# Kernel tuning notes

Measured on AMD Instinct MI355X. Metric: run time of the kernel, lower is better.

## Reference

```python
import jax, jax.numpy as jnp
import numpy as np

IN_CH, OUT_CH, HID = 16, 16, 64
POS_DIM = 3
N_POINTS = 50000
N_EDGES = 800000
BATCH = 1

def setup_inputs() -> dict:
    key = jax.random.key(0)
    ks = jax.random.split(key, 10)
    x = jax.random.normal(ks[0], (BATCH, N_POINTS, IN_CH), dtype=jnp.float32)
    pos = jax.random.uniform(ks[1], (N_POINTS, POS_DIM), dtype=jnp.float32)
    edge_index = jax.random.randint(ks[2], (2, N_EDGES), 0, N_POINTS, dtype=jnp.int64)
    def lin(k, fan_in, fan_out):
        kw, kb = jax.random.split(k)
        bound = 1.0 / np.sqrt(fan_in)
        W = jax.random.uniform(kw, (fan_in, fan_out), minval=-bound, maxval=bound, dtype=jnp.float32)
        b = jax.random.uniform(kb, (fan_out,), minval=-bound, maxval=bound, dtype=jnp.float32)
        return W, b
    W1, b1 = lin(ks[3], 2 * POS_DIM, HID)
    Wh, bh = lin(ks[4], HID, HID)
    Wo, bo = lin(ks[5], HID, IN_CH * OUT_CH)
    return {"x": x, "pos": pos, "edge_index": edge_index,
            "W1": W1, "b1": b1, "Wh": Wh, "bh": bh, "Wo": Wo, "bo": bo}

def reference(x, pos, edge_index, W1, b1, Wh, bh, Wo, bo):
    gelu = lambda t: jax.nn.gelu(t, approximate=False)  # matches torch F.gelu default
    batch_size, n_points, in_ch = x.shape
    pos_flat = jnp.broadcast_to(pos[None], (batch_size,) + pos.shape).reshape(-1, pos.shape[-1])
    x_flat = x.reshape(-1, in_ch)
    src, dst = edge_index[0], edge_index[1]
    pos_enc = jnp.concatenate([pos_flat[src], pos_flat[dst]], axis=-1)  # [E, 2*pos_dim]
    h = gelu(pos_enc @ W1 + b1)
    h = gelu(h @ Wh + bh)
    h = h @ Wo + bo                                  # [E, in*out]
    kernel_weights = h.reshape(-1, in_ch, OUT_CH)    # [E, in, out]
    msg = jnp.einsum('eio,ei->eo', kernel_weights, x_flat[src])  # [E, out]
    out_flat = jax.ops.segment_sum(msg, dst, num_segments=batch_size * n_points)
    return out_flat.reshape(batch_size, n_points, OUT_CH)
```

## Files before the change

kernel.cpp:

```cpp
#include <hip/hip_runtime.h>

#define NPTS   50000
#define NEDGE  800000
#define NTILES 50000
#define NPAIRS 25000
#define NBLK   768
#define TOTW   (NBLK * 8)

typedef short  bf16x8 __attribute__((ext_vector_type(8)));
typedef float  f32x4  __attribute__((ext_vector_type(4)));
typedef int    i32x4  __attribute__((ext_vector_type(4)));
typedef unsigned short u16x8 __attribute__((ext_vector_type(8)));

__device__ __forceinline__ float gelu_tanh(float v) {
    float v2 = v * v;
    float u2 = v * fmaf(v2, 0.0713548162726f, 1.5957691216057f);
    float e  = __expf(u2);
    float r  = __builtin_amdgcn_rcpf(e + 1.0f);
    return v - v * r;
}

__device__ __forceinline__ short f2bf(float f) {
    unsigned u = __builtin_bit_cast(unsigned, f);
    unsigned r = (u + 0x7FFFu + ((u >> 16) & 1u)) >> 16;
    return (short)r;
}
__device__ __forceinline__ float bf2f(unsigned short h) {
    return __builtin_bit_cast(float, (unsigned)h << 16);
}

__device__ __forceinline__ int cvt_pk_bf16(float a, float b) {
    int r;
    asm("v_cvt_pk_bf16_f32 %0, %1, %2" : "=v"(r) : "v"(a), "v"(b));
    return r;
}

__device__ __forceinline__ int bperm(int addr, int v) {
    return __builtin_amdgcn_ds_bpermute(addr, v);
}
__device__ __forceinline__ int fbits(float v) { return __builtin_bit_cast(int, v); }
__device__ __forceinline__ float ibits(int v) { return __builtin_bit_cast(float, v); }

__global__ void zero_out_kernel(float* __restrict__ out, int n) {
    int i = blockIdx.x * blockDim.x + threadIdx.x;
    if (i < n) out[i] = 0.0f;
}

__global__ void xcopy_kernel(const float* __restrict__ x, unsigned short* __restrict__ xbf) {
    int i = blockIdx.x * 256 + threadIdx.x;
    if (i >= (NPTS * 16) / 4) return;
    float4 v = reinterpret_cast<const float4*>(x)[i];
    ushort4 o;
    o.x = (unsigned short)f2bf(v.x);
    o.y = (unsigned short)f2bf(v.y);
    o.z = (unsigned short)f2bf(v.z);
    o.w = (unsigned short)f2bf(v.w);
    reinterpret_cast<ushort4*>(xbf)[i] = o;
}

__global__ __launch_bounds__(512, 4) void edge_mfma_kernel(
    const unsigned short* __restrict__ xbf,
    const float* __restrict__ pos,
    const int*   __restrict__ ei,
    const float* __restrict__ W1,
    const float* __restrict__ b1,
    const float* __restrict__ Wh,
    const float* __restrict__ bh,
    const float* __restrict__ Wo,
    const float* __restrict__ bo,
    float* __restrict__ out)
{
    __shared__ bf16x8 WoF[32][64];
    __shared__ bf16x8 WhF[8][64];
    __shared__ bf16x8 W1F[4][64];
    __shared__ bf16x8 BOF[64];
    __shared__ float  bhs[64];

    const int tid = threadIdx.x;

#pragma unroll
    for (int p = 0; p < 4; ++p) {
        int e_id = p * 512 + tid;
        int s  = e_id >> 6;
        int l  = e_id & 63;
        int er_ = l & 15, g = l >> 4;
        int i  = s >> 1, kt = s & 1;
        int n  = i * 16 + er_;
        int kb = kt * 32 + g * 8;
        bf16x8 f;
#pragma unroll
        for (int j = 0; j < 8; ++j)
            f[j] = f2bf(Wo[(kb + j) * 256 + n]);
        WoF[s][l] = f;
    }
    {
        int s  = tid >> 6;
        int l  = tid & 63;
        int er_ = l & 15, g = l >> 4;
        int m  = s >> 1, kt = s & 1;
        int n  = m * 16 + er_;
        int kb = kt * 32 + g * 8;
        bf16x8 f;
#pragma unroll
        for (int j = 0; j < 8; ++j)
            f[j] = f2bf(Wh[(kb + j) * 64 + n]);
        WhF[s][l] = f;
    }
    if (tid < 256) {
        int m  = tid >> 6;
        int l  = tid & 63;
        int er_ = l & 15, g = l >> 4;
        int n  = m * 16 + er_;
        bf16x8 f;
#pragma unroll
        for (int j = 0; j < 8; ++j) {
            int k = g * 8 + j;
            float v = (k < 6) ? W1[k * 64 + n] : (k == 6 ? b1[n] : 0.0f);
            f[j] = f2bf(v);
        }
        W1F[m][l] = f;
    }
    if (tid < 64) {
        int er_ = tid & 15, g = tid >> 4;
        bf16x8 f;
#pragma unroll
        for (int j = 0; j < 8; ++j) {
            int i = g * 8 + j;
            f[j] = (g < 2) ? f2bf(bo[i * 16 + er_]) : (short)0;
        }
        BOF[tid] = f;
        bhs[tid] = bh[tid];
    }
    __syncthreads();

    const int wave = tid >> 6;
    const int lane = tid & 63;
    const int grp  = lane >> 4;
    const int er   = lane & 15;

    const int addrH0 = (er + (grp & 1) * 32) * 4;
    const int addrH1 = addrH0 + 64;
    const bool selHi = (grp >= 2);
    int addrT[4], addrD[4];
#pragma unroll
    for (int r = 0; r < 4; ++r) {
        addrT[r] = ((er >> 2) * 16 + grp * 4 + r) * 4;
        addrD[r] = (grp * 4 + r) * 4;
    }
    const int selT = er & 3;

    const bf16x8* wof = &WoF[0][lane];
    const bf16x8* whf = &WhF[0][lane];
    const bf16x8* w1f = &W1F[0][lane];
    const bf16x8  bofr = BOF[lane];
    const f32x4 zero = {0.f, 0.f, 0.f, 0.f};

    const int gwave = blockIdx.x * 8 + wave;

#pragma unroll 1
    for (int pr = gwave; pr < NPAIRS; pr += TOTW) {
        int sQ[2], dQ[2];
        bf16x8 apeQ[2];
        u16x8 xA[2], xB[2];
#pragma unroll
        for (int q = 0; q < 2; ++q) {
            const int eb = (2 * pr + q) << 4;
            int s = ei[eb + er];
            int d = ei[NEDGE + eb + er];
            s = min(max(s, 0), NPTS - 1);
            d = min(max(d, 0), NPTS - 1);
            sQ[q] = s; dQ[q] = d;

            const u16x8* xp = reinterpret_cast<const u16x8*>(xbf + (size_t)s * 16);
            xA[q] = xp[0];
            xB[q] = xp[1];

            float p0 = pos[s * 3 + 0], p1 = pos[s * 3 + 1], p2 = pos[s * 3 + 2];
            float p3 = pos[d * 3 + 0], p4 = pos[d * 3 + 1], p5 = pos[d * 3 + 2];
            const bool g0 = (grp == 0);
            bf16x8 ap;
            ap[0] = g0 ? f2bf(p0) : (short)0;
            ap[1] = g0 ? f2bf(p1) : (short)0;
            ap[2] = g0 ? f2bf(p2) : (short)0;
            ap[3] = g0 ? f2bf(p3) : (short)0;
            ap[4] = g0 ? f2bf(p4) : (short)0;
            ap[5] = g0 ? f2bf(p5) : (short)0;
            ap[6] = g0 ? (short)0x3F80 : (short)0;
            ap[7] = 0;
            apeQ[q] = ap;
        }

        float g1[2][4][4];
#pragma unroll
        for (int q = 0; q < 2; ++q)
#pragma unroll
            for (int m = 0; m < 4; ++m) {
                f32x4 c = __builtin_amdgcn_mfma_f32_16x16x32_bf16(w1f[m * 64], apeQ[q], zero, 0, 0, 0);
#pragma unroll
                for (int r = 0; r < 4; ++r) g1[q][m][r] = gelu_tanh(c[r]);
            }

        bf16x8 B2[2][2];
#pragma unroll
        for (int q = 0; q < 2; ++q)
#pragma unroll
            for (int kt = 0; kt < 2; ++kt) {
                int pk0[2], pk1[2];
#pragma unroll
                for (int rp = 0; rp < 2; ++rp) {
                    pk0[rp] = cvt_pk_bf16(g1[q][2 * kt + 0][2 * rp], g1[q][2 * kt + 0][2 * rp + 1]);
                    pk1[rp] = cvt_pk_bf16(g1[q][2 * kt + 1][2 * rp], g1[q][2 * kt + 1][2 * rp + 1]);
                }
                i32x4 w;
#pragma unroll
                for (int h = 0; h < 2; ++h) {
                    int ah = h ? addrH1 : addrH0;
#pragma unroll
                    for (int rp = 0; rp < 2; ++rp) {
                        int vA = bperm(ah, pk0[rp]);
                        int vB = bperm(ah, pk1[rp]);
                        w[h * 2 + rp] = selHi ? vB : vA;
                    }
                }
                B2[q][kt] = __builtin_bit_cast(bf16x8, w);
            }

        float g2[2][4][4];
#pragma unroll
        for (int q = 0; q < 2; ++q)
#pragma unroll
            for (int m = 0; m < 4; ++m) {
                f32x4 c = __builtin_amdgcn_mfma_f32_16x16x32_bf16(whf[(2 * m + 0) * 64], B2[q][0], zero, 0, 0, 0);
                c = __builtin_amdgcn_mfma_f32_16x16x32_bf16(whf[(2 * m + 1) * 64], B2[q][1], c, 0, 0, 0);
                float4 b4 = *reinterpret_cast<const float4*>(&bhs[m * 16 + grp * 4]);
                float bb[4] = {b4.x, b4.y, b4.z, b4.w};
#pragma unroll
                for (int r = 0; r < 4; ++r) g2[q][m][r] = gelu_tanh(c[r] + bb[r]);
            }

        bf16x8 B3[2][2];
#pragma unroll
        for (int q = 0; q < 2; ++q)
#pragma unroll
            for (int kt = 0; kt < 2; ++kt) {
                int pk0[2], pk1[2];
#pragma unroll
                for (int rp = 0; rp < 2; ++rp) {
                    pk0[rp] = cvt_pk_bf16(g2[q][2 * kt + 0][2 * rp], g2[q][2 * kt + 0][2 * rp + 1]);
                    pk1[rp] = cvt_pk_bf16(g2[q][2 * kt + 1][2 * rp], g2[q][2 * kt + 1][2 * rp + 1]);
                }
                i32x4 w;
#pragma unroll
                for (int h = 0; h < 2; ++h) {
                    int ah = h ? addrH1 : addrH0;
#pragma unroll
                    for (int rp = 0; rp < 2; ++rp) {
                        int vA = bperm(ah, pk0[rp]);
                        int vB = bperm(ah, pk1[rp]);
                        w[h * 2 + rp] = selHi ? vB : vA;
                    }
                }
                B3[q][kt] = __builtin_bit_cast(bf16x8, w);
            }

        f32x4 msg[2];
#pragma unroll
        for (int q = 0; q < 2; ++q) {
            bf16x8 xb;
#pragma unroll
            for (int j = 0; j < 8; ++j) {
                short v = (grp == 0) ? (short)xA[q][j] : ((grp == 1) ? (short)xB[q][j] : (short)0);
                xb[j] = v;
            }
            msg[q] = __builtin_amdgcn_mfma_f32_16x16x32_bf16(bofr, xb, zero, 0, 0, 0);
        }

#pragma unroll
        for (int i = 0; i < 16; ++i)
#pragma unroll
            for (int q = 0; q < 2; ++q) {
                f32x4 c = __builtin_amdgcn_mfma_f32_16x16x32_bf16(wof[(2 * i + 0) * 64], B3[q][0], zero, 0, 0, 0);
                c = __builtin_amdgcn_mfma_f32_16x16x32_bf16(wof[(2 * i + 1) * 64], B3[q][1], c, 0, 0, 0);
                float xf = bf2f(i < 8 ? xA[q][i] : xB[q][i - 8]);
#pragma unroll
                for (int r = 0; r < 4; ++r)
                    msg[q][r] = fmaf(xf, c[r], msg[q][r]);
            }

#pragma unroll
        for (int q = 0; q < 2; ++q) {
#pragma unroll
            for (int rd = 0; rd < 4; ++rd) {
                int u0 = bperm(addrT[rd], fbits(msg[q][0]));
                int u1 = bperm(addrT[rd], fbits(msg[q][1]));
                int u2 = bperm(addrT[rd], fbits(msg[q][2]));
                int u3 = bperm(addrT[rd], fbits(msg[q][3]));
                int v  = (selT == 0) ? u0 : (selT == 1) ? u1 : (selT == 2) ? u2 : u3;
                int dv = bperm(addrD[rd], dQ[q]);
                atomicAdd(out + (size_t)dv * 16 + er, ibits(v));
            }
        }
    }
}

extern "C" void kernel_launch(void* const* d_in, const int* in_sizes, int n_in,
                              void* d_out, int out_size, void* d_ws, size_t ws_size,
                              hipStream_t stream) {
    const float* x   = (const float*)d_in[0];
    const float* pos = (const float*)d_in[1];
    const int*   ei  = (const int*)d_in[2];
    const float* W1  = (const float*)d_in[3];
    const float* b1  = (const float*)d_in[4];
    const float* Wh  = (const float*)d_in[5];
    const float* bh  = (const float*)d_in[6];
    const float* Wo  = (const float*)d_in[7];
    const float* bo  = (const float*)d_in[8];
    float* out = (float*)d_out;
    unsigned short* xbf = (unsigned short*)d_ws;

    zero_out_kernel<<<(out_size + 255) / 256, 256, 0, stream>>>(out, out_size);
    xcopy_kernel<<<((NPTS * 16 / 4) + 255) / 256, 256, 0, stream>>>(x, xbf);
    edge_mfma_kernel<<<NBLK, 512, 0, stream>>>(
        xbf, pos, ei, W1, b1, Wh, bh, Wo, bo, out);
}
```

Baseline: 170.0 us.

## Pack per-node bf16 x and pos records, fuse prep kernels, add dynamic work queue

Fuses the output-zeroing and x-to-bf16 conversion into one prep kernel. That kernel also writes a 64-byte per-node record holding bf16 features and bf16 positions, so each edge gathers a node's data from one cache line instead of separate fp32 pos loads. The fixed strided split of edge pairs across waves is replaced by a global atomic counter that hands out pairs dynamically, prefetching the next index to balance load. This adds one global atomic per pair and a larger workspace footprint.

```diff
diff --git a/kernel.cpp b/kernel.cpp
--- a/kernel.cpp
+++ b/kernel.cpp
@@ -5,7 +5,7 @@
 #define NTILES 50000
 #define NPAIRS 25000
 #define NBLK   768
-#define TOTW   (NBLK * 8)
+#define WS_CNT (NPTS * 64)
 
 typedef short  bf16x8 __attribute__((ext_vector_type(8)));
 typedef float  f32x4  __attribute__((ext_vector_type(4)));
@@ -20,10 +20,10 @@
     return v - v * r;
 }
 
-__device__ __forceinline__ short f2bf(float f) {
+__device__ __forceinline__ unsigned short f2bf(float f) {
     unsigned u = __builtin_bit_cast(unsigned, f);
     unsigned r = (u + 0x7FFFu + ((u >> 16) & 1u)) >> 16;
-    return (short)r;
+    return (unsigned short)r;
 }
 __device__ __forceinline__ float bf2f(unsigned short h) {
     return __builtin_bit_cast(float, (unsigned)h << 16);
@@ -41,26 +41,30 @@
 __device__ __forceinline__ int fbits(float v) { return __builtin_bit_cast(int, v); }
 __device__ __forceinline__ float ibits(int v) { return __builtin_bit_cast(float, v); }
 
-__global__ void zero_out_kernel(float* __restrict__ out, int n) {
-    int i = blockIdx.x * blockDim.x + threadIdx.x;
-    if (i < n) out[i] = 0.0f;
-}
-
-__global__ void xcopy_kernel(const float* __restrict__ x, unsigned short* __restrict__ xbf) {
+__global__ void prep_kernel(const float* __restrict__ x, const float* __restrict__ pos,
+                            float* __restrict__ out, unsigned short* __restrict__ nrec,
+                            int* __restrict__ cnt) {
     int i = blockIdx.x * 256 + threadIdx.x;
-    if (i >= (NPTS * 16) / 4) return;
-    float4 v = reinterpret_cast<const float4*>(x)[i];
-    ushort4 o;
-    o.x = (unsigned short)f2bf(v.x);
-    o.y = (unsigned short)f2bf(v.y);
-    o.z = (unsigned short)f2bf(v.z);
-    o.w = (unsigned short)f2bf(v.w);
-    reinterpret_cast<ushort4*>(xbf)[i] = o;
+    if (i == 0) *cnt = 0;
+    if (i < NPTS * 16) out[i] = 0.0f;
+    if (i < NPTS) {
+        const float4* xp = reinterpret_cast<const float4*>(x + (size_t)i * 16);
+        float4 a = xp[0], b = xp[1], c = xp[2], d = xp[3];
+        u16x8 r0, r1, r2, r3;
+        r0[0]=f2bf(a.x); r0[1]=f2bf(a.y); r0[2]=f2bf(a.z); r0[3]=f2bf(a.w);
+        r0[4]=f2bf(b.x); r0[5]=f2bf(b.y); r0[6]=f2bf(b.z); r0[7]=f2bf(b.w);
+        r1[0]=f2bf(c.x); r1[1]=f2bf(c.y); r1[2]=f2bf(c.z); r1[3]=f2bf(c.w);
+        r1[4]=f2bf(d.x); r1[5]=f2bf(d.y); r1[6]=f2bf(d.z); r1[7]=f2bf(d.w);
+        r2[0]=f2bf(pos[i*3+0]); r2[1]=f2bf(pos[i*3+1]); r2[2]=f2bf(pos[i*3+2]);
+        r2[3]=0; r2[4]=0; r2[5]=0; r2[6]=0; r2[7]=0;
+        r3[0]=0; r3[1]=0; r3[2]=0; r3[3]=0; r3[4]=0; r3[5]=0; r3[6]=0; r3[7]=0;
+        u16x8* dst = reinterpret_cast<u16x8*>(nrec + (size_t)i * 32);
+        dst[0] = r0; dst[1] = r1; dst[2] = r2; dst[3] = r3;
+    }
 }
 
 __global__ __launch_bounds__(512, 4) void edge_mfma_kernel(
-    const unsigned short* __restrict__ xbf,
-    const float* __restrict__ pos,
+    const unsigned short* __restrict__ nrec,
     const int*   __restrict__ ei,
     const float* __restrict__ W1,
     const float* __restrict__ b1,
@@ -68,7 +72,8 @@
     const float* __restrict__ bh,
     const float* __restrict__ Wo,
     const float* __restrict__ bo,
-    float* __restrict__ out)
+    float* __restrict__ out,
+    int* __restrict__ cnt)
 {
     __shared__ bf16x8 WoF[32][64];
     __shared__ bf16x8 WhF[8][64];
@@ -90,7 +95,7 @@
         bf16x8 f;
 #pragma unroll
         for (int j = 0; j < 8; ++j)
-            f[j] = f2bf(Wo[(kb + j) * 256 + n]);
+            f[j] = (short)f2bf(Wo[(kb + j) * 256 + n]);
         WoF[s][l] = f;
     }
     {
@@ -103,7 +108,7 @@
         bf16x8 f;
 #pragma unroll
         for (int j = 0; j < 8; ++j)
-            f[j] = f2bf(Wh[(kb + j) * 64 + n]);
+            f[j] = (short)f2bf(Wh[(kb + j) * 64 + n]);
         WhF[s][l] = f;
     }
     if (tid < 256) {
@@ -116,7 +121,7 @@
         for (int j = 0; j < 8; ++j) {
             int k = g * 8 + j;
             float v = (k < 6) ? W1[k * 64 + n] : (k == 6 ? b1[n] : 0.0f);
-            f[j] = f2bf(v);
+            f[j] = (short)f2bf(v);
         }
         W1F[m][l] = f;
     }
@@ -126,7 +131,7 @@
 #pragma unroll
         for (int j = 0; j < 8; ++j) {
             int i = g * 8 + j;
-            f[j] = (g < 2) ? f2bf(bo[i * 16 + er_]) : (short)0;
+            f[j] = (g < 2) ? (short)f2bf(bo[i * 16 + er_]) : (short)0;
         }
         BOF[tid] = f;
         bhs[tid] = bh[tid];
@@ -155,11 +160,24 @@
     const bf16x8  bofr = BOF[lane];
     const f32x4 zero = {0.f, 0.f, 0.f, 0.f};
 
-    const int gwave = blockIdx.x * 8 + wave;
+    int myp;
+    {
+        int v = 0;
+        if (lane == 0) v = atomicAdd(cnt, 1);
+        myp = __builtin_amdgcn_readfirstlane(v);
+    }
 
 #pragma unroll 1
-    for (int pr = gwave; pr < NPAIRS; pr += TOTW) {
-        int sQ[2], dQ[2];
+    while (myp < NPAIRS) {
+        int nxt;
+        {
+            int v = 0;
+            if (lane == 0) v = atomicAdd(cnt, 1);
+            nxt = __builtin_amdgcn_readfirstlane(v);
+        }
+        const int pr = myp;
+
+        int dQ[2];
         bf16x8 apeQ[2];
         u16x8 xA[2], xB[2];
 #pragma unroll
@@ -169,22 +187,22 @@
             int d = ei[NEDGE + eb + er];
             s = min(max(s, 0), NPTS - 1);
             d = min(max(d, 0), NPTS - 1);
-            sQ[q] = s; dQ[q] = d;
-
-            const u16x8* xp = reinterpret_cast<const u16x8*>(xbf + (size_t)s * 16);
-            xA[q] = xp[0];
-            xB[q] = xp[1];
-
-            float p0 = pos[s * 3 + 0], p1 = pos[s * 3 + 1], p2 = pos[s * 3 + 2];
-            float p3 = pos[d * 3 + 0], p4 = pos[d * 3 + 1], p5 = pos[d * 3 + 2];
+            dQ[q] = d;
+
+            const u16x8* rp = reinterpret_cast<const u16x8*>(nrec + (size_t)s * 32);
+            xA[q] = rp[0];
+            xB[q] = rp[1];
+            ushort4 ps = *reinterpret_cast<const ushort4*>(nrec + (size_t)s * 32 + 16);
+            ushort4 pd = *reinterpret_cast<const ushort4*>(nrec + (size_t)d * 32 + 16);
+
             const bool g0 = (grp == 0);
             bf16x8 ap;
-            ap[0] = g0 ? f2bf(p0) : (short)0;
-            ap[1] = g0 ? f2bf(p1) : (short)0;
-            ap[2] = g0 ? f2bf(p2) : (short)0;
-            ap[3] = g0 ? f2bf(p3) : (short)0;
-            ap[4] = g0 ? f2bf(p4) : (short)0;
-            ap[5] = g0 ? f2bf(p5) : (short)0;
+            ap[0] = g0 ? (short)ps.x : (short)0;
+            ap[1] = g0 ? (short)ps.y : (short)0;
+            ap[2] = g0 ? (short)ps.z : (short)0;
+            ap[3] = g0 ? (short)pd.x : (short)0;
+            ap[4] = g0 ? (short)pd.y : (short)0;
+            ap[5] = g0 ? (short)pd.z : (short)0;
             ap[6] = g0 ? (short)0x3F80 : (short)0;
             ap[7] = 0;
             apeQ[q] = ap;
@@ -300,6 +318,8 @@
                 atomicAdd(out + (size_t)dv * 16 + er, ibits(v));
             }
         }
+
+        myp = nxt;
     }
 }
 
@@ -316,10 +336,11 @@
     const float* Wo  = (const float*)d_in[7];
     const float* bo  = (const float*)d_in[8];
     float* out = (float*)d_out;
-    unsigned short* xbf = (unsigned short*)d_ws;
-
-    zero_out_kernel<<<(out_size + 255) / 256, 256, 0, stream>>>(out, out_size);
-    xcopy_kernel<<<((NPTS * 16 / 4) + 255) / 256, 256, 0, stream>>>(x, xbf);
+
+    unsigned short* nrec = (unsigned short*)d_ws;
+    int* cnt = (int*)((char*)d_ws + WS_CNT);
+
+    prep_kernel<<<(NPTS * 16 + 255) / 256, 256, 0, stream>>>(x, pos, out, nrec, cnt);
     edge_mfma_kernel<<<NBLK, 512, 0, stream>>>(
-        xbf, pos, ei, W1, b1, Wh, bh, Wo, bo, out);
-}
+        nrec, ei, W1, b1, Wh, bh, Wo, bo, out, cnt);
+}
```

Result: slower. 456.4 us (+168.5%).
